# Performance work log

Measured on AMD Instinct MI355X. Metric: run time of the kernel, lower is better.

Reference implementation:

```python
import jax, jax.numpy as jnp
import numpy as np

NH, DK, DV, D = 8, 64, 64, 768
DECAY = 0.95
WRITE_STRENGTH = 0.1


def setup_inputs() -> dict:
    key = jax.random.key(0)
    ks = jax.random.split(key, 6)
    s = 0.02  # small init scale for projection weights
    return {
        "x": jax.random.normal(ks[0], (4, 4096, D), dtype=jnp.float32),
        "w_key": jax.random.normal(ks[1], (NH * DK, D), dtype=jnp.float32) * s,
        "w_value": jax.random.normal(ks[2], (NH * DV, D), dtype=jnp.float32) * s,
        "w_query": jax.random.normal(ks[3], (NH * DK, D), dtype=jnp.float32) * s,
        "w_gate": jax.random.normal(ks[4], (NH, D), dtype=jnp.float32) * s,
        "w_out": jax.random.normal(ks[5], (D, NH * DV), dtype=jnp.float32) * s,
    }


def reference(x, w_key, w_value, w_query, w_gate, w_out):
    B, S, _ = x.shape
    # Batched projections (torch Linear: y = x @ W.T)
    k = (x @ w_key.T).reshape(B, S, NH, DK)
    v = (x @ w_value.T).reshape(B, S, NH, DV)
    q = (x @ w_query.T).reshape(B, S, NH, DK)
    gate = jax.nn.sigmoid(x @ w_gate.T)  # (B, S, NH)

    # Writes only use batch element 0 (mirrors k[0], v[0], gate[0] in source)
    k0 = k[0]      # (S, NH, DK)
    v0 = v[0]      # (S, NH, DV)
    g0 = gate[0]   # (S, NH)

    def step(fw, inp):
        q_t, k0_t, v0_t, g0_t = inp
        # Read BEFORE this step's decay+write
        retrieved = jnp.einsum('bhk,hkv->bhv', q_t, fw)  # (B, NH, DV)
        write = (WRITE_STRENGTH * g0_t)[:, None, None] * (k0_t[:, :, None] * v0_t[:, None, :])
        fw_new = DECAY * fw + jax.lax.stop_gradient(write)
        return fw_new, retrieved

    fw0 = jnp.zeros((NH, DK, DV), dtype=x.dtype)
    inputs = (q.transpose(1, 0, 2, 3), k0, v0, g0)  # time-major
    _, retrieved = jax.lax.scan(step, fw0, inputs)   # (S, B, NH, DV)
    retrieved = retrieved.transpose(1, 0, 2, 3).reshape(B, S, NH * DV)
    return x + retrieved @ w_out.T
```

## Files before the change

kernel.cpp:

```cpp
#include <hip/hip_runtime.h>
#include <hip/hip_bf16.h>

typedef __hip_bfloat16 bf16;
typedef __attribute__((ext_vector_type(8))) short   bf16x8;
typedef __attribute__((ext_vector_type(4))) float   f32x4;

#define B_   4
#define S_   4096
#define D_   768
#define NH_  8
#define DK_  64
#define DV_  64
#define CH_  64
#define NCH_ (S_/CH_)
#define DECAY_ 0.95f
#define WSTR_  0.1f

__device__ __forceinline__ float b2f(bf16 v) { return __bfloat162float(v); }
__device__ __forceinline__ bf16  f2b(float v) { return __float2bfloat16(v); }

__device__ __forceinline__ void gl2lds16(const bf16* g, bf16* lds) {
    __builtin_amdgcn_global_load_lds(
        (const __attribute__((address_space(1))) void*)g,
        (__attribute__((address_space(3))) void*)lds, 16, 0, 0);
}

__global__ __launch_bounds__(192) void cast_fused(const float* __restrict__ x,
                                                  bf16* __restrict__ xb,
                                                  const float* __restrict__ wg,
                                                  float* __restrict__ wgt,
                                                  const float* __restrict__ wq,
                                                  const float* __restrict__ wk,
                                                  const float* __restrict__ wv,
                                                  const float* __restrict__ wo,
                                                  bf16* __restrict__ dq, bf16* __restrict__ dk,
                                                  bf16* __restrict__ dv, bf16* __restrict__ dob) {
    const int tid = threadIdx.x;
    if (blockIdx.x >= (B_ * S_)) {
        const int idx = blockIdx.x - B_ * S_;
        const int which = idx >> 9, b = idx & 511;
        const float* src = which == 0 ? wq : which == 1 ? wk : which == 2 ? wv : wo;
        bf16*       dst = which == 0 ? dq : which == 1 ? dk : which == 2 ? dv : dob;
        const int i = (b * 192 + tid) * 4;
        const float4 v = *reinterpret_cast<const float4*>(src + i);
        union { bf16 b4[4]; ushort4 u; } t;
        t.b4[0] = f2b(v.x); t.b4[1] = f2b(v.y); t.b4[2] = f2b(v.z); t.b4[3] = f2b(v.w);
        *reinterpret_cast<ushort4*>(dst + i) = t.u;
        return;
    }
    const int s = blockIdx.x;
    const float4 v = *reinterpret_cast<const float4*>(x + (size_t)s * D_ + tid * 4);
    union { bf16 b4[4]; ushort4 u; } t;
    t.b4[0] = f2b(v.x); t.b4[1] = f2b(v.y); t.b4[2] = f2b(v.z); t.b4[3] = f2b(v.w);
    *reinterpret_cast<ushort4*>(xb + (size_t)s * D_ + tid * 4) = t.u;

    if (s < S_) {
        __shared__ float red[3 * 8];
        float p[8];
        const float* wgp = wg + tid * 4;
        #pragma unroll
        for (int h = 0; h < 8; h++) {
            const float4 wv4 = *reinterpret_cast<const float4*>(wgp + h * D_);
            p[h] = v.x * wv4.x + v.y * wv4.y + v.z * wv4.z + v.w * wv4.w;
        }
        #pragma unroll
        for (int h = 0; h < 8; h++)
            #pragma unroll
            for (int off = 32; off; off >>= 1) p[h] += __shfl_down(p[h], off);
        const int w = tid >> 6, lane = tid & 63;
        if (lane == 0) {
            #pragma unroll
            for (int h = 0; h < 8; h++) red[w * 8 + h] = p[h];
        }
        __syncthreads();
        if (tid < 8) {
            const float sum = red[tid] + red[8 + tid] + red[16 + tid];
            wgt[s * NH_ + tid] = WSTR_ / (1.f + expf(-sum));
        }
    }
}

template<typename TC, int ADDX, int NITER>
__device__ __forceinline__ void gemm_body(bf16* As, bf16* Bs,
                                          const bf16* __restrict__ A,
                                          const bf16* __restrict__ Bm,
                                          const float* __restrict__ X,
                                          TC* __restrict__ C,
                                          int bm, int bn, int K, int N) {
    const int tid = threadIdx.x, lane = tid & 63, w = tid >> 6;
    const int quad = lane >> 4, l16 = lane & 15;
    const int wm = (w >> 1) * 64, wn = (w & 1) * 64;
    const int lrow = lane >> 3;
    const int lcol = ((lane & 7) ^ lrow) * 8;

    f32x4 acc[4][4] = {};

    for (int it = 0; it < NITER; it++) {
        const int k0 = it * 64;
        #pragma unroll
        for (int c = 0; c < 4; c++) {
            const int seg = w * 4 + c;
            const int row = seg * 8 + lrow;
            gl2lds16(A  + (size_t)(bm + row) * K + k0 + lcol, &As[seg * 512]);
            gl2lds16(Bm + (size_t)(bn + row) * K + k0 + lcol, &Bs[seg * 512]);
        }
        __syncthreads();
        #pragma unroll
        for (int kh = 0; kh < 2; kh++) {
            bf16x8 af[4], bfr[4];
            #pragma unroll
            for (int t = 0; t < 4; t++) {
                const int cb = ((kh * 4 + quad) ^ (l16 & 7)) * 8;
                af[t]  = *reinterpret_cast<const bf16x8*>(&As[(wm + t * 16 + l16) * 64 + cb]);
                bfr[t] = *reinterpret_cast<const bf16x8*>(&Bs[(wn + t * 16 + l16) * 64 + cb]);
            }
            #pragma unroll
            for (int mt = 0; mt < 4; mt++)
                #pragma unroll
                for (int nt = 0; nt < 4; nt++)
                    acc[mt][nt] = __builtin_amdgcn_mfma_f32_16x16x32_bf16(
                        af[mt], bfr[nt], acc[mt][nt], 0, 0, 0);
        }
        __syncthreads();
    }

    #pragma unroll
    for (int mt = 0; mt < 4; mt++)
        #pragma unroll
        for (int nt = 0; nt < 4; nt++)
            #pragma unroll
            for (int r = 0; r < 4; r++) {
                const int m = bm + wm + mt * 16 + quad * 4 + r;
                const int n = bn + wn + nt * 16 + l16;
                float v = acc[mt][nt][r];
                if (ADDX) v += X[(size_t)m * N + n];
                if (sizeof(TC) == 2) *(bf16*)&C[(size_t)m * N + n] = f2b(v);
                else                 *(float*)&C[(size_t)m * N + n] = v;
            }
}

__global__ __launch_bounds__(256) void proj_fused(const bf16* __restrict__ xb,
                                                  const bf16* __restrict__ wqb,
                                                  const bf16* __restrict__ wkb,
                                                  const bf16* __restrict__ wvb,
                                                  bf16* __restrict__ qbuf,
                                                  bf16* __restrict__ k0buf,
                                                  bf16* __restrict__ v0buf) {
    __shared__ bf16 As[128 * 64];
    __shared__ bf16 Bs[128 * 64];
    const int id = blockIdx.x;
    const int xcd = id & 7;
    int j = id >> 3;
    const bf16* Bm; bf16* C; int bm, bn;
    if (j < 64) {
        bm = (xcd + ((j >> 2) << 3)) * 128;
        bn = (j & 3) * 128;
        Bm = wqb; C = qbuf;
    } else {
        j -= 64;
        bm = (xcd + ((j >> 3) << 3)) * 128;
        const int b8 = j & 7;
        bn = (b8 & 3) * 128;
        Bm = (b8 < 4) ? wkb : wvb;
        C  = (b8 < 4) ? k0buf : v0buf;
    }
    gemm_body<bf16, 0, 12>(As, Bs, xb, Bm, nullptr, C, bm, bn, D_, 512);
}

__global__ __launch_bounds__(256) void gemm_out(const bf16* __restrict__ retr,
                                                const bf16* __restrict__ wob,
                                                const float* __restrict__ x,
                                                float* __restrict__ out) {
    __shared__ bf16 As[128 * 64];
    __shared__ bf16 Bs[128 * 64];
    const int gx = gridDim.x, gy = gridDim.y;
    const int L = blockIdx.y * gx + blockIdx.x;
    const int rpx = gy >> 3;
    const int xcd = L & 7;
    const int i   = L >> 3;
    const int by = xcd * rpx + i / gx;
    const int bx = i % gx;
    gemm_body<float, 1, 8>(As, Bs, retr, wob, x, out, by * 128, bx * 128, 512, D_);
}

__global__ __launch_bounds__(256) void chunk_sums(const bf16* __restrict__ k0,
                                                  const bf16* __restrict__ v0,
                                                  const float* __restrict__ wgt,
                                                  bf16* __restrict__ lsumsT) {
    const int n = blockIdx.x, h = blockIdx.y;
    __shared__ float ks[CH_][65];
    __shared__ float vs[CH_][64];
    __shared__ float cw[CH_];
    const int tid = threadIdx.x;
    for (int e = tid; e < CH_ * 64; e += 256) {
        const int r = e >> 6, c = e & 63;
        const int t = n * CH_ + r;
        ks[r][c] = b2f(k0[(size_t)t * (NH_ * DK_) + h * DK_ + c]);
        vs[r][c] = b2f(v0[(size_t)t * (NH_ * DV_) + h * DV_ + c]);
    }
    if (tid < CH_) {
        const int t = n * CH_ + tid;
        cw[tid] = powf(DECAY_, (float)(CH_ - 1 - tid)) * wgt[t * NH_ + h];
    }
    __syncthreads();
    const int j = tid & 63, ig = tid >> 6;
    float acc[16] = {};
    for (int idx = 0; idx < CH_; idx++) {
        const float ck = cw[idx] * ks[idx][j];
        #pragma unroll
        for (int r = 0; r < 16; r++) acc[r] += vs[idx][ig * 16 + r] * ck;
    }
    bf16* outp = lsumsT + ((size_t)(n * NH_ + h)) * (DK_ * DV_);
    #pragma unroll
    for (int r = 0; r < 16; r++) outp[(ig * 16 + r) * 64 + j] = f2b(acc[r]);
}

__device__ __forceinline__ void cvt4(ushort4 u, float f[4]) {
    union { unsigned u; float f; } c;
    c.u = (unsigned)u.x << 16; f[0] = c.f;
    c.u = (unsigned)u.y << 16; f[1] = c.f;
    c.u = (unsigned)u.z << 16; f[2] = c.f;
    c.u = (unsigned)u.w << 16; f[3] = c.f;
}

__global__ __launch_bounds__(256) void chunk_output(const bf16* __restrict__ q,
                                                    const bf16* __restrict__ k0,
                                                    const bf16* __restrict__ v0,
                                                    const float* __restrict__ wgt,
                                                    const bf16* __restrict__ lsumsT,
                                                    bf16* __restrict__ retr) {
    const int n = blockIdx.x, h = blockIdx.y;
    __shared__ bf16 QsAm[4][64 * 64];
    __shared__ bf16 Ks[64 * 64];
    __shared__ bf16 FWT[64 * 64];
    __shared__ bf16 VT[64 * 72];
    __shared__ float dpow[64], winv[64];
    const int tid = threadIdx.x, lane = tid & 63, w = tid >> 6;
    const int quad = lane >> 4, l16 = lane & 15;
    const int t0 = n * CH_;
    const int lrow = lane >> 3;
    const int lcol = ((lane & 7) ^ lrow) * 8;

    #pragma unroll
    for (int seg = 0; seg < 8; seg++) {
        const int row = seg * 8 + lrow;
        gl2lds16(q + ((size_t)(w * S_ + t0 + row)) * 512 + h * 64 + lcol, &QsAm[w][seg * 512]);
    }
    #pragma unroll
    for (int c = 0; c < 2; c++) {
        const int seg = w * 2 + c;
        const int row = seg * 8 + lrow;
        gl2lds16(k0 + ((size_t)(t0 + row)) * 512 + h * 64 + lcol, &Ks[seg * 512]);
    }

    {
        float fwacc[16] = {};
        const float dcp[4] = { 1.0f, 0.0375241f, 1.40806e-3f, 5.28365e-5f };
        #pragma unroll
        for (int jj = 1; jj <= 4; jj++) {
            const int nm = n - jj;
            if (nm < 0) break;
            const ushort* Lp = (const ushort*)(lsumsT + ((size_t)(nm * NH_ + h)) * 4096) + tid * 16;
            #pragma unroll
            for (int u = 0; u < 4; u++) {
                float f[4];
                cvt4(reinterpret_cast<const ushort4*>(Lp)[u], f);
                #pragma unroll
                for (int e = 0; e < 4; e++) fwacc[u * 4 + e] += dcp[jj - 1] * f[e];
            }
        }
        const int frow = tid >> 2;
        #pragma unroll
        for (int half = 0; half < 2; half++) {
            const int cb = (tid & 3) * 2 + half;
            union { bf16 b8v[8]; bf16x8 v; } t;
            #pragma unroll
            for (int e = 0; e < 8; e++) t.b8v[e] = f2b(fwacc[half * 8 + e]);
            *reinterpret_cast<bf16x8*>(&FWT[frow * 64 + (cb ^ (frow & 7)) * 8]) = t.v;
        }
    }
    {
        ushort4 vreg[4];
        const int jb = (tid & 15) * 4;
        const int sb = tid >> 4;
        #pragma unroll
        for (int it = 0; it < 4; it++)
            vreg[it] = *reinterpret_cast<const ushort4*>(
                v0 + ((size_t)(t0 + sb + it * 16)) * 512 + h * 64 + jb);
        ushort* VTu = reinterpret_cast<ushort*>(VT);
        #pragma unroll
        for (int it = 0; it < 4; it++) {
            const int s = sb + it * 16;
            VTu[(jb + 0) * 72 + s] = vreg[it].x;
            VTu[(jb + 1) * 72 + s] = vreg[it].y;
            VTu[(jb + 2) * 72 + s] = vreg[it].z;
            VTu[(jb + 3) * 72 + s] = vreg[it].w;
        }
    }
    if (tid < 64) {
        dpow[tid] = powf(DECAY_, (float)tid);
        winv[tid] = wgt[(t0 + tid) * NH_ + h] * powf(DECAY_, -(float)(tid + 1));
    }
    __syncthreads();

    const int cb0 = ((quad) ^ (l16 & 7)) * 8;
    const int cb1 = ((4 + quad) ^ (l16 & 7)) * 8;
    bf16* Qw = &QsAm[w][0];

    bf16x8 af[4][2];
    #pragma unroll
    for (int mt = 0; mt < 4; mt++) {
        af[mt][0] = *reinterpret_cast<const bf16x8*>(&Qw[(mt * 16 + l16) * 64 + cb0]);
        af[mt][1] = *reinterpret_cast<const bf16x8*>(&Qw[(mt * 16 + l16) * 64 + cb1]);
    }

    f32x4 acc[4][4] = {};
    #pragma unroll
    for (int kh = 0; kh < 2; kh++) {
        bf16x8 bk[4];
        #pragma unroll
        for (int nt = 0; nt < 4; nt++)
            bk[nt] = *reinterpret_cast<const bf16x8*>(
                &Ks[(nt * 16 + l16) * 64 + (kh ? cb1 : cb0)]);
        #pragma unroll
        for (int mt = 0; mt < 4; mt++)
            #pragma unroll
            for (int nt = 0; nt < 4; nt++)
                acc[mt][nt] = __builtin_amdgcn_mfma_f32_16x16x32_bf16(
                    af[mt][kh], bk[nt], acc[mt][nt], 0, 0, 0);
    }

    const float pmt[4] = { 1.0f, 0.4401266694f, 0.1937114891f, 0.0852578070f };
    const f32x4 dpb = *reinterpret_cast<const f32x4*>(&dpow[quad * 4]);
    float winv_l[4];
    #pragma unroll
    for (int nt = 0; nt < 4; nt++) winv_l[nt] = winv[nt * 16 + l16];
    #pragma unroll
    for (int mt = 0; mt < 4; mt++)
        #pragma unroll
        for (int nt = 0; nt < 4; nt++)
            #pragma unroll
            for (int r = 0; r < 4; r++) {
                const int tt = mt * 16 + quad * 4 + r;
                const int s = nt * 16 + l16;
                const float v = (s < tt) ? acc[mt][nt][r] * (dpb[r] * pmt[mt]) * winv_l[nt] : 0.f;
                Qw[tt * 64 + (((s >> 3) ^ (tt & 7)) << 3) + (s & 7)] = f2b(v);
            }

    f32x4 o[4][4] = {};
    #pragma unroll
    for (int kh = 0; kh < 2; kh++) {
        bf16x8 ff[4];
        #pragma unroll
        for (int nt = 0; nt < 4; nt++)
            ff[nt] = *reinterpret_cast<const bf16x8*>(
                &FWT[(nt * 16 + l16) * 64 + (kh ? cb1 : cb0)]);
        #pragma unroll
        for (int mt = 0; mt < 4; mt++)
            #pragma unroll
            for (int nt = 0; nt < 4; nt++)
                o[mt][nt] = __builtin_amdgcn_mfma_f32_16x16x32_bf16(
                    af[mt][kh], ff[nt], o[mt][nt], 0, 0, 0);
    }
    #pragma unroll
    for (int mt = 0; mt < 4; mt++)
        #pragma unroll
        for (int nt = 0; nt < 4; nt++)
            #pragma unroll
            for (int r = 0; r < 4; r++) o[mt][nt][r] *= dpb[r] * pmt[mt];

    #pragma unroll
    for (int kh = 0; kh < 2; kh++) {
        bf16x8 am[4], vf[4];
        #pragma unroll
        for (int mt = 0; mt < 4; mt++)
            am[mt] = *reinterpret_cast<const bf16x8*>(
                &Qw[(mt * 16 + l16) * 64 + (kh ? cb1 : cb0)]);
        #pragma unroll
        for (int nt = 0; nt < 4; nt++)
            vf[nt] = *reinterpret_cast<const bf16x8*>(
                &VT[(nt * 16 + l16) * 72 + kh * 32 + quad * 8]);
        #pragma unroll
        for (int mt = 0; mt < 4; mt++)
            #pragma unroll
            for (int nt = 0; nt < 4; nt++)
                o[mt][nt] = __builtin_amdgcn_mfma_f32_16x16x32_bf16(
                    am[mt], vf[nt], o[mt][nt], 0, 0, 0);
    }

    #pragma unroll
    for (int mt = 0; mt < 4; mt++)
        #pragma unroll
        for (int nt = 0; nt < 4; nt++)
            #pragma unroll
            for (int r = 0; r < 4; r++) {
                const int tt = mt * 16 + quad * 4 + r;
                retr[((size_t)(w * S_ + t0 + tt)) * 512 + h * 64 + nt * 16 + l16] =
                    f2b(o[mt][nt][r]);
            }
}

extern "C" void kernel_launch(void* const* d_in, const int* in_sizes, int n_in,
                              void* d_out, int out_size, void* d_ws, size_t ws_size,
                              hipStream_t stream) {
    const float* x  = (const float*)d_in[0];
    const float* wk = (const float*)d_in[1];
    const float* wv = (const float*)d_in[2];
    const float* wq = (const float*)d_in[3];
    const float* wg = (const float*)d_in[4];
    const float* wo = (const float*)d_in[5];
    float* out = (float*)d_out;

    const size_t MB1 = 1ull << 20;
    char* w = (char*)d_ws;
    bf16*  qbuf    = (bf16*)(w);
    bf16*  k0buf   = (bf16*)(w + 16 * MB1);
    bf16*  v0buf   = (bf16*)(w + 20 * MB1);
    float* wgt     = (float*)(w + 24 * MB1);
    bf16*  wqb     = (bf16*)(w + 24 * MB1 + (128ull<<10));
    bf16*  wkb     = (bf16*)(w + 24 * MB1 + (128ull<<10) + 1*786432);
    bf16*  wvb     = (bf16*)(w + 24 * MB1 + (128ull<<10) + 2*786432);
    bf16*  wob     = (bf16*)(w + 24 * MB1 + (128ull<<10) + 3*786432);
    bf16*  lsumsT  = (bf16*)(w + 28 * MB1);
    bf16*  retr    = (bf16*)(w + 32 * MB1);
    bf16*  xb      = (bf16*)(w + 48 * MB1);

    const int MB = B_ * S_;

    cast_fused<<<MB + 2048, 192, 0, stream>>>(x, xb, wg, wgt,
                                              wq, wk, wv, wo, wqb, wkb, wvb, wob);

    proj_fused<<<768, 256, 0, stream>>>(xb, wqb, wkb, wvb, qbuf, k0buf, v0buf);

    chunk_sums<<<dim3(NCH_, NH_), 256, 0, stream>>>(k0buf, v0buf, wgt, lsumsT);
    chunk_output<<<dim3(NCH_, NH_), 256, 0, stream>>>(qbuf, k0buf, v0buf, wgt, lsumsT, retr);

    gemm_out<<<dim3(D_ / 128, MB / 128), 256, 0, stream>>>(retr, wob, x, out);
}
```

Measured before the change: 196.2 us.

## Double-buffer LDS tiles in the shared GEMM body to overlap loads with MFMA

Turns the shared GEMM mainloop into a two-stage pipeline. The next K-tile is loaded into a second LDS buffer with global_load_lds while MFMAs run on the current one, using explicit vmcnt waits and raw s_barrier in place of two __syncthreads per iteration. The aim is to hide global load latency in both the projection and output GEMMs. LDS per block doubles to 64KB, which may lower occupancy, and the vmcnt(8) count must match the 8 loads issued per stage exactly.

New measurement: 186.0 us. 5.2% less time.

```diff
diff --git a/kernel.cpp b/kernel.cpp
--- a/kernel.cpp
+++ b/kernel.cpp
@@ -95,24 +95,41 @@
 
     f32x4 acc[4][4] = {};
 
-    for (int it = 0; it < NITER; it++) {
+    auto STAGE = [&](int it, int buf) {
         const int k0 = it * 64;
+        bf16* Ad = As + buf * 8192;
+        bf16* Bd = Bs + buf * 8192;
         #pragma unroll
         for (int c = 0; c < 4; c++) {
             const int seg = w * 4 + c;
             const int row = seg * 8 + lrow;
-            gl2lds16(A  + (size_t)(bm + row) * K + k0 + lcol, &As[seg * 512]);
-            gl2lds16(Bm + (size_t)(bn + row) * K + k0 + lcol, &Bs[seg * 512]);
-        }
-        __syncthreads();
+            gl2lds16(A  + (size_t)(bm + row) * K + k0 + lcol, &Ad[seg * 512]);
+            gl2lds16(Bm + (size_t)(bn + row) * K + k0 + lcol, &Bd[seg * 512]);
+        }
+    };
+
+    STAGE(0, 0);
+    for (int it = 0; it < NITER; ++it) {
+        const int cur = it & 1;
+        if (it + 1 < NITER) {
+            STAGE(it + 1, cur ^ 1);
+            asm volatile("s_waitcnt vmcnt(8)" ::: "memory");
+        } else {
+            asm volatile("s_waitcnt vmcnt(0)" ::: "memory");
+        }
+        __builtin_amdgcn_s_barrier();
+        asm volatile("" ::: "memory");
+
+        const bf16* Ar = As + cur * 8192;
+        const bf16* Br = Bs + cur * 8192;
         #pragma unroll
         for (int kh = 0; kh < 2; kh++) {
             bf16x8 af[4], bfr[4];
             #pragma unroll
             for (int t = 0; t < 4; t++) {
                 const int cb = ((kh * 4 + quad) ^ (l16 & 7)) * 8;
-                af[t]  = *reinterpret_cast<const bf16x8*>(&As[(wm + t * 16 + l16) * 64 + cb]);
-                bfr[t] = *reinterpret_cast<const bf16x8*>(&Bs[(wn + t * 16 + l16) * 64 + cb]);
+                af[t]  = *reinterpret_cast<const bf16x8*>(&Ar[(wm + t * 16 + l16) * 64 + cb]);
+                bfr[t] = *reinterpret_cast<const bf16x8*>(&Br[(wn + t * 16 + l16) * 64 + cb]);
             }
             #pragma unroll
             for (int mt = 0; mt < 4; mt++)
@@ -121,7 +138,10 @@
                     acc[mt][nt] = __builtin_amdgcn_mfma_f32_16x16x32_bf16(
                         af[mt], bfr[nt], acc[mt][nt], 0, 0, 0);
         }
-        __syncthreads();
+        if (it + 1 < NITER) {
+            asm volatile("" ::: "memory");
+            __builtin_amdgcn_s_barrier();
+        }
     }
 
     #pragma unroll
@@ -146,8 +166,8 @@
                                                   bf16* __restrict__ qbuf,
                                                   bf16* __restrict__ k0buf,
                                                   bf16* __restrict__ v0buf) {
-    __shared__ bf16 As[128 * 64];
-    __shared__ bf16 Bs[128 * 64];
+    __shared__ bf16 As[2 * 128 * 64];
+    __shared__ bf16 Bs[2 * 128 * 64];
     const int id = blockIdx.x;
     const int xcd = id & 7;
     int j = id >> 3;
@@ -171,8 +191,8 @@
                                                 const bf16* __restrict__ wob,
                                                 const float* __restrict__ x,
                                                 float* __restrict__ out) {
-    __shared__ bf16 As[128 * 64];
-    __shared__ bf16 Bs[128 * 64];
+    __shared__ bf16 As[2 * 128 * 64];
+    __shared__ bf16 Bs[2 * 128 * 64];
     const int gx = gridDim.x, gy = gridDim.y;
     const int L = blockIdx.y * gx + blockIdx.x;
     const int rpx = gy >> 3;
```
